# Performance work log

Measured on AMD Instinct MI355X. Metric: run time of the kernel, lower is better.

## Reference

```python
import jax, jax.numpy as jnp
import numpy as np

B, S, D, H = 2, 2048, 1024, 16
HD = D // H
NEG = -10000.0


def setup_inputs() -> dict:
    key = jax.random.key(0)
    ks = jax.random.split(key, 9)
    # xavier-uniform-like scale for square d_model x d_model weights
    lim = float(np.sqrt(6.0 / (D + D)))
    mk_w = lambda k: jax.random.uniform(k, (D, D), jnp.float32, -lim, lim)
    return {
        "q": jax.random.normal(ks[0], (B, S, D), jnp.float32),
        "k": jax.random.normal(ks[1], (B, S, D), jnp.float32),
        "v": jax.random.normal(ks[2], (B, S, D), jnp.float32),
        "attn_mask": jax.random.randint(ks[3], (B, S), 0, 2, jnp.int32),
        "Wq": mk_w(ks[4]),
        "Wk": mk_w(ks[5]),
        "Wv": mk_w(ks[6]),
        "Wo": mk_w(ks[7]),
        "mask_future": 1,
    }


def reference(q, k, v, attn_mask, Wq, Wk, Wv, Wo, mask_future):
    # nn.Linear(bias=False): y = x @ W.T
    def split_heads(x, W):
        return (x @ W.T).reshape(B, S, H, HD).transpose(0, 2, 1, 3)  # [B,H,S,HD]

    qh = split_heads(q, Wq)
    kh = split_heads(k, Wk)
    vh = split_heads(v, Wv)

    scale = 1.0 / np.sqrt(HD)
    scores = jnp.einsum("bhld,bhsd->bhls", qh, kh) * scale  # [B,H,L,S]

    if mask_future:  # static python flag
        rows = jnp.arange(S)[:, None]
        cols = jnp.arange(S)[None, :]
        causal_bias = jnp.where(cols > rows, jnp.float32(NEG), jnp.float32(0.0))
        scores = scores + causal_bias

    # masked_fill(attn_mask == 0, -10000): sets score exactly to NEG (after bias add)
    pad = attn_mask[:, None, None, :]  # [B,1,1,S]
    scores = jnp.where(pad == 0, jnp.float32(NEG), scores)

    probs = jax.nn.softmax(scores, axis=-1)
    ctx = jnp.einsum("bhls,bhsd->bhld", probs, vh)  # [B,H,L,HD]
    ctx = ctx.transpose(0, 2, 1, 3).reshape(B, S, D)
    return ctx @ Wo.T
```

## Files before the change

kernel.cpp:

```cpp
#include <hip/hip_runtime.h>
#include <hip/hip_bf16.h>

typedef __attribute__((ext_vector_type(8))) short bf16x8;
typedef __attribute__((ext_vector_type(4))) short bf16x4;
typedef __attribute__((ext_vector_type(4))) float f32x4;

#define B_ 2
#define S_ 2048
#define D_ 1024
#define H_ 16
#define HD_ 64
#define M_ 4096
#define NEGV (-10000.0f)

#define NQ_ 4194304
#define NW_ 1048576

#if __has_builtin(__builtin_amdgcn_mfma_f32_16x16x16bf16_1k)
#define HAVE_MFMA16 1
#else
#define HAVE_MFMA16 0
#endif

static __device__ __forceinline__ unsigned short f2bf(float x) {
  __hip_bfloat16 h = __float2bfloat16(x);
  return *reinterpret_cast<unsigned short*>(&h);
}

static __device__ __forceinline__ bf16x8 cvt8(const float* p) {
  float4 a = *reinterpret_cast<const float4*>(p);
  float4 b = *reinterpret_cast<const float4*>(p + 4);
  bf16x8 r;
  r[0] = (short)f2bf(a.x); r[1] = (short)f2bf(a.y);
  r[2] = (short)f2bf(a.z); r[3] = (short)f2bf(a.w);
  r[4] = (short)f2bf(b.x); r[5] = (short)f2bf(b.y);
  r[6] = (short)f2bf(b.z); r[7] = (short)f2bf(b.w);
  return r;
}

static __device__ __forceinline__ void gl_lds16(const unsigned short* g, unsigned short* l) {
#if __has_builtin(__builtin_amdgcn_global_load_lds)
  __builtin_amdgcn_global_load_lds(
      (const __attribute__((address_space(1))) unsigned int*)g,
      (__attribute__((address_space(3))) unsigned int*)l, 16, 0, 0);
#else
  *reinterpret_cast<bf16x8*>(l) = *reinterpret_cast<const bf16x8*>(g);
#endif
}


__global__ __launch_bounds__(256) void cvt_all(const float* __restrict__ q,
                                               const float* __restrict__ k,
                                               const float* __restrict__ v,
                                               const float* __restrict__ wq,
                                               const float* __restrict__ wk,
                                               const float* __restrict__ wv,
                                               const float* __restrict__ wo,
                                               unsigned short* __restrict__ dst) {
  for (size_t c = (size_t)blockIdx.x * 256 + threadIdx.x; c < 2097152; c += (size_t)2048 * 256) {
    const size_t e = c * 8;
    const float* s;
    if (e < (size_t)NQ_)            s = q  + e;
    else if (e < (size_t)2 * NQ_)   s = k  + (e - (size_t)NQ_);
    else if (e < (size_t)3 * NQ_)   s = v  + (e - (size_t)2 * NQ_);
    else if (e < (size_t)3 * NQ_ + NW_)     s = wq + (e - (size_t)3 * NQ_);
    else if (e < (size_t)3 * NQ_ + 2 * NW_) s = wk + (e - (size_t)3 * NQ_ - NW_);
    else if (e < (size_t)3 * NQ_ + 3 * NW_) s = wv + (e - (size_t)3 * NQ_ - 2 * NW_);
    else                                    s = wo + (e - (size_t)3 * NQ_ - 3 * NW_);
    *reinterpret_cast<bf16x8*>(dst + e) = cvt8(s);
  }
}

template<bool HSPLIT>
static __device__ __forceinline__ void core_fast(const unsigned short* A,
                                                 const unsigned short* Bw,
                                                 unsigned short* Asm, unsigned short* Bsm,
                                                 int m0, int n0, f32x4 (*acc)[4]) {
  const int tid = threadIdx.x, lane = tid & 63, wid = tid >> 6;
  const int wm = wid >> 1, wn = wid & 1;
  const int l15 = lane & 15, l4 = lane >> 4;

  for (int k0 = 0; k0 < 1024; k0 += 64) {
    __syncthreads();
#pragma unroll
    for (int i = 0; i < 4; ++i) {
      const int idx = tid + 256 * i;
      const int row = idx >> 3;
      const int ce = ((idx & 7) * 8) ^ ((row & 7) << 3);
      const unsigned short* ga;
      if constexpr (HSPLIT) {
        const int m = m0 + row, kk = k0 + ce;
        const int bb = m >> 11, s = m & 2047;
        ga = A + (((size_t)(bb * H_ + (kk >> 6)) * S_ + s) * HD_ + (kk & 63));
      } else {
        ga = A + (size_t)(m0 + row) * 1024 + k0 + ce;
      }
      gl_lds16(ga, Asm + (size_t)idx * 8);
      gl_lds16(Bw + (size_t)(n0 + row) * 1024 + k0 + ce, Bsm + (size_t)idx * 8);
    }
    __syncthreads();
#pragma unroll
    for (int kk = 0; kk < 2; ++kk) {
      bf16x8 af[4], bfr[4];
#pragma unroll
      for (int f = 0; f < 4; ++f) {
        const int ra = wm * 64 + f * 16 + l15;
        const int ca = (kk * 32 + l4 * 8) ^ ((ra & 7) << 3);
        af[f] = *reinterpret_cast<const bf16x8*>(&Asm[ra * 64 + ca]);
        const int rb = wn * 64 + f * 16 + l15;
        const int cb = (kk * 32 + l4 * 8) ^ ((rb & 7) << 3);
        bfr[f] = *reinterpret_cast<const bf16x8*>(&Bsm[rb * 64 + cb]);
      }
#pragma unroll
      for (int fm = 0; fm < 4; ++fm)
#pragma unroll
        for (int fn = 0; fn < 4; ++fn)
          acc[fm][fn] = __builtin_amdgcn_mfma_f32_16x16x32_bf16(af[fm], bfr[fn], acc[fm][fn], 0, 0, 0);
    }
  }
}

__global__ __launch_bounds__(256) void gemm_qkv_fast(const unsigned short* __restrict__ qbf,
                                                     const unsigned short* __restrict__ kbf,
                                                     const unsigned short* __restrict__ vbf,
                                                     const unsigned short* __restrict__ wbf,
                                                     unsigned short* __restrict__ Qh,
                                                     unsigned short* __restrict__ Kh,
                                                     unsigned short* __restrict__ Vt) {
  __shared__ unsigned short Asm[128 * 64];
  __shared__ unsigned short Bsm[128 * 64];
  const int z = blockIdx.z;
  const unsigned short* A  = (z == 0) ? qbf : (z == 1) ? kbf : vbf;
  const unsigned short* Bw = wbf + (size_t)z * NW_;
  const int m0 = blockIdx.y * 128, n0 = blockIdx.x * 128;
  const int lane = threadIdx.x & 63, wid = threadIdx.x >> 6;
  const int wm = wid >> 1, wn = wid & 1;
  const int l15 = lane & 15, l4 = lane >> 4;
  f32x4 acc[4][4] = {};
  core_fast<false>(A, Bw, Asm, Bsm, m0, n0, acc);

#pragma unroll
  for (int fm = 0; fm < 4; ++fm) {
#pragma unroll
    for (int fn = 0; fn < 4; ++fn) {
      const int mg0 = m0 + wm * 64 + fm * 16 + l4 * 4;
      const int ng  = n0 + wn * 64 + fn * 16 + l15;
      const int bidx = mg0 >> 11, s = mg0 & 2047;
      const int h = ng >> 6, d = ng & 63;
      if (z < 2) {
        unsigned short* C = (z == 0) ? Qh : Kh;
#pragma unroll
        for (int r = 0; r < 4; ++r)
          C[((size_t)((bidx * H_ + h) * S_ + s + r)) * HD_ + d] = f2bf(acc[fm][fn][r]);
      } else {
        ushort4 pk;
        pk.x = f2bf(acc[fm][fn][0]); pk.y = f2bf(acc[fm][fn][1]);
        pk.z = f2bf(acc[fm][fn][2]); pk.w = f2bf(acc[fm][fn][3]);
        *reinterpret_cast<ushort4*>(&Vt[((size_t)((bidx * H_ + h) * HD_ + d)) * S_ + s]) = pk;
      }
    }
  }
}

__global__ __launch_bounds__(256) void gemm_o_fast(const unsigned short* __restrict__ ctx,
                                                   const unsigned short* __restrict__ wobf,
                                                   float* __restrict__ Cout) {
  __shared__ unsigned short Asm[128 * 64];
  __shared__ unsigned short Bsm[128 * 64];
  const int m0 = blockIdx.y * 128, n0 = blockIdx.x * 128;
  const int lane = threadIdx.x & 63, wid = threadIdx.x >> 6;
  const int wm = wid >> 1, wn = wid & 1;
  const int l15 = lane & 15, l4 = lane >> 4;
  f32x4 acc[4][4] = {};
  core_fast<true>(ctx, wobf, Asm, Bsm, m0, n0, acc);

#pragma unroll
  for (int fm = 0; fm < 4; ++fm)
#pragma unroll
    for (int fn = 0; fn < 4; ++fn) {
      const int mg0 = m0 + wm * 64 + fm * 16 + l4 * 4;
      const int ng  = n0 + wn * 64 + fn * 16 + l15;
#pragma unroll
      for (int r = 0; r < 4; ++r)
        Cout[(size_t)(mg0 + r) * 1024 + ng] = acc[fm][fn][r];
    }
}


template<bool AF32, bool BF32, bool HSPLIT>
static __device__ __forceinline__ void gemm_core(const void* Av, const void* Bv,
                                                 unsigned short* Asm, unsigned short* Bsm,
                                                 int m0, int n0, f32x4 (*acc)[4]) {
  constexpr int BK = 64, LDT = 72;
  constexpr int K = 1024;
  const int tid = threadIdx.x;
  const int lane = tid & 63, wid = tid >> 6;
  const int wm = wid >> 1, wn = wid & 1;
  const int l15 = lane & 15, l4 = lane >> 4;

  for (int k0 = 0; k0 < K; k0 += BK) {
    __syncthreads();
#pragma unroll
    for (int i = 0; i < 4; ++i) {
      int idx = tid + 256 * i;
      int row = idx >> 3, k8 = (idx & 7) * 8;
      bf16x8 va, vb;
      if constexpr (AF32) {
        va = cvt8((const float*)Av + (size_t)(m0 + row) * K + k0 + k8);
      } else if constexpr (HSPLIT) {
        const int m = m0 + row, kk = k0 + k8;
        const int bb = m >> 11, s = m & 2047;
        va = *reinterpret_cast<const bf16x8*>(
            (const unsigned short*)Av +
            (((size_t)(bb * H_ + (kk >> 6)) * S_ + s) * HD_ + (kk & 63)));
      } else {
        va = *reinterpret_cast<const bf16x8*>((const unsigned short*)Av + (size_t)(m0 + row) * K + k0 + k8);
      }
      if constexpr (BF32) {
        vb = cvt8((const float*)Bv + (size_t)(n0 + row) * K + k0 + k8);
      } else {
        vb = *reinterpret_cast<const bf16x8*>((const unsigned short*)Bv + (size_t)(n0 + row) * K + k0 + k8);
      }
      *reinterpret_cast<bf16x8*>(&Asm[row * LDT + k8]) = va;
      *reinterpret_cast<bf16x8*>(&Bsm[row * LDT + k8]) = vb;
    }
    __syncthreads();
#pragma unroll
    for (int kk = 0; kk < 2; ++kk) {
      bf16x8 af[4], bfr[4];
#pragma unroll
      for (int f = 0; f < 4; ++f) {
        af[f]  = *reinterpret_cast<const bf16x8*>(&Asm[(wm * 64 + f * 16 + l15) * LDT + kk * 32 + l4 * 8]);
        bfr[f] = *reinterpret_cast<const bf16x8*>(&Bsm[(wn * 64 + f * 16 + l15) * LDT + kk * 32 + l4 * 8]);
      }
#pragma unroll
      for (int fm = 0; fm < 4; ++fm)
#pragma unroll
        for (int fn = 0; fn < 4; ++fn)
          acc[fm][fn] = __builtin_amdgcn_mfma_f32_16x16x32_bf16(af[fm], bfr[fn], acc[fm][fn], 0, 0, 0);
    }
  }
}

__global__ __launch_bounds__(256) void gemm_qkv3(const float* __restrict__ q,
                                                 const float* __restrict__ k,
                                                 const float* __restrict__ v,
                                                 const float* __restrict__ Wq,
                                                 const float* __restrict__ Wk,
                                                 const float* __restrict__ Wv,
                                                 unsigned short* __restrict__ Qh,
                                                 unsigned short* __restrict__ Kh,
                                                 unsigned short* __restrict__ Vt) {
  constexpr int LDT = 72;
  __shared__ unsigned short Asm[128 * LDT];
  __shared__ unsigned short Bsm[128 * LDT];
  const int z = blockIdx.z;
  const float* A  = (z == 0) ? q  : (z == 1) ? k  : v;
  const float* Bw = (z == 0) ? Wq : (z == 1) ? Wk : Wv;
  const int m0 = blockIdx.y * 128, n0 = blockIdx.x * 128;
  const int lane = threadIdx.x & 63, wid = threadIdx.x >> 6;
  const int wm = wid >> 1, wn = wid & 1;
  const int l15 = lane & 15, l4 = lane >> 4;
  f32x4 acc[4][4] = {};
  gemm_core<true, true, false>(A, Bw, Asm, Bsm, m0, n0, acc);

#pragma unroll
  for (int fm = 0; fm < 4; ++fm) {
#pragma unroll
    for (int fn = 0; fn < 4; ++fn) {
      const int mg0 = m0 + wm * 64 + fm * 16 + l4 * 4;
      const int ng  = n0 + wn * 64 + fn * 16 + l15;
      const int bidx = mg0 >> 11, s = mg0 & 2047;
      const int h = ng >> 6, d = ng & 63;
      if (z < 2) {
        unsigned short* C = (z == 0) ? Qh : Kh;
#pragma unroll
        for (int r = 0; r < 4; ++r)
          C[((size_t)((bidx * H_ + h) * S_ + s + r)) * HD_ + d] = f2bf(acc[fm][fn][r]);
      } else {
        ushort4 pk;
        pk.x = f2bf(acc[fm][fn][0]); pk.y = f2bf(acc[fm][fn][1]);
        pk.z = f2bf(acc[fm][fn][2]); pk.w = f2bf(acc[fm][fn][3]);
        *reinterpret_cast<ushort4*>(&Vt[((size_t)((bidx * H_ + h) * HD_ + d)) * S_ + s]) = pk;
      }
    }
  }
}

__global__ __launch_bounds__(256) void gemm_oproj(const void* __restrict__ Av,
                                                  const void* __restrict__ Bv,
                                                  float* __restrict__ Cout) {
  constexpr int LDT = 72;
  __shared__ unsigned short Asm[128 * LDT];
  __shared__ unsigned short Bsm[128 * LDT];
  const int m0 = blockIdx.y * 128, n0 = blockIdx.x * 128;
  const int lane = threadIdx.x & 63, wid = threadIdx.x >> 6;
  const int wm = wid >> 1, wn = wid & 1;
  const int l15 = lane & 15, l4 = lane >> 4;
  f32x4 acc[4][4] = {};
  gemm_core<false, true, true>(Av, Bv, Asm, Bsm, m0, n0, acc);

#pragma unroll
  for (int fm = 0; fm < 4; ++fm)
#pragma unroll
    for (int fn = 0; fn < 4; ++fn) {
      const int mg0 = m0 + wm * 64 + fm * 16 + l4 * 4;
      const int ng  = n0 + wn * 64 + fn * 16 + l15;
#pragma unroll
      for (int r = 0; r < 4; ++r)
        Cout[(size_t)(mg0 + r) * 1024 + ng] = acc[fm][fn][r];
    }
}

__global__ __launch_bounds__(128) void attn_fwd(const unsigned short* Qh,
                                                const unsigned short* __restrict__ Kh,
                                                const unsigned short* __restrict__ Vt,
                                                const int* __restrict__ attn_mask,
                                                const int* __restrict__ mask_future,
                                                unsigned short* ctx) {
  constexpr int KVB = 64;
  __shared__ unsigned short Ksm[64 * 64];
  __shared__ unsigned short Vsm[64 * 64];
#if !HAVE_MFMA16
  __shared__ unsigned short Psm[2][16 * 72];
#endif
  __shared__ int s_any;
  const int tid = threadIdx.x, lane = tid & 63, wid = tid >> 6;
  const int l15 = lane & 15, l4 = lane >> 4;
  const int bh = blockIdx.y, b = bh >> 4;
  const int q0 = (int)((blockIdx.x + 9 * blockIdx.y) & 31) * 64;
  const bool causal = (mask_future[0] != 0);
  const int* mrow = attn_mask + b * S_;

  if (tid == 0) s_any = 0;
  __syncthreads();
  for (int i = tid; i <= q0; i += 128)
    if (mrow[i]) s_any = 1;
  __syncthreads();
  const int kb_end = (causal && s_any) ? (q0 + 64) : S_;

  const unsigned short* Qb = Qh + (size_t)bh * S_ * HD_;
  const unsigned short* Kb = Kh + (size_t)bh * S_ * HD_;
  const unsigned short* Vb = Vt + (size_t)bh * HD_ * S_;

  int qrow[2];
  bf16x8 qf0[2], qf1[2];
#pragma unroll
  for (int f = 0; f < 2; ++f) {
    qrow[f] = q0 + wid * 32 + f * 16 + l15;
    qf0[f] = *reinterpret_cast<const bf16x8*>(&Qb[(size_t)qrow[f] * HD_ + l4 * 8]);
    qf1[f] = *reinterpret_cast<const bf16x8*>(&Qb[(size_t)qrow[f] * HD_ + 32 + l4 * 8]);
  }

  float m_run[2] = {-1e30f, -1e30f}, l_run[2] = {0.f, 0.f};
  f32x4 o[2][4] = {};

  bf16x8 kreg[4], vreg[4];
#pragma unroll
  for (int j = 0; j < 4; ++j) {
    const int idx = tid + 128 * j;
    const int row = idx >> 3;
    const int ce = ((idx & 7) * 8) ^ ((row & 7) << 3);
    kreg[j] = *reinterpret_cast<const bf16x8*>(&Kb[(size_t)row * HD_ + ce]);
    vreg[j] = *reinterpret_cast<const bf16x8*>(&Vb[(size_t)row * S_ + ce]);
  }

  for (int kb = 0; kb < kb_end; kb += KVB) {
    __syncthreads();
#pragma unroll
    for (int j = 0; j < 4; ++j) {
      const int idx = tid + 128 * j;
      *reinterpret_cast<bf16x8*>(&Ksm[idx * 8]) = kreg[j];
      *reinterpret_cast<bf16x8*>(&Vsm[idx * 8]) = vreg[j];
    }
    __syncthreads();

    if (kb + KVB < kb_end) {
      const int kn = kb + KVB;
#pragma unroll
      for (int j = 0; j < 4; ++j) {
        const int idx = tid + 128 * j;
        const int row = idx >> 3;
        const int ce = ((idx & 7) * 8) ^ ((row & 7) << 3);
        kreg[j] = *reinterpret_cast<const bf16x8*>(&Kb[(size_t)(kn + row) * HD_ + ce]);
        vreg[j] = *reinterpret_cast<const bf16x8*>(&Vb[(size_t)row * S_ + kn + ce]);
      }
    }

    int4 mk4[4];
#pragma unroll
    for (int nf = 0; nf < 4; ++nf)
      mk4[nf] = *reinterpret_cast<const int4*>(&mrow[kb + nf * 16 + l4 * 4]);

#pragma unroll
    for (int f = 0; f < 2; ++f) {
      f32x4 sc[4];
#pragma unroll
      for (int nf = 0; nf < 4; ++nf) {
        const int ra = nf * 16 + l15, sw = (ra & 7) << 3;
        bf16x8 kf0 = *reinterpret_cast<const bf16x8*>(&Ksm[ra * 64 + ((l4 * 8) ^ sw)]);
        bf16x8 kf1 = *reinterpret_cast<const bf16x8*>(&Ksm[ra * 64 + ((32 + l4 * 8) ^ sw)]);
        f32x4 z = {};
        z = __builtin_amdgcn_mfma_f32_16x16x32_bf16(kf0, qf0[f], z, 0, 0, 0);
        z = __builtin_amdgcn_mfma_f32_16x16x32_bf16(kf1, qf1[f], z, 0, 0, 0);
        sc[nf] = z;
      }

      float p[4][4];
      float mx = -1e30f;
#pragma unroll
      for (int nf = 0; nf < 4; ++nf) {
        const int kbase = kb + nf * 16 + l4 * 4;
#pragma unroll
        for (int r = 0; r < 4; ++r) {
          float vv = sc[nf][r] * 0.125f;
          if (causal && (kbase + r) > qrow[f]) vv += NEGV;
          const int mkr = (r == 0) ? mk4[nf].x : (r == 1) ? mk4[nf].y : (r == 2) ? mk4[nf].z : mk4[nf].w;
          if (mkr == 0) vv = NEGV;
          p[nf][r] = vv;
          mx = fmaxf(mx, vv);
        }
      }
      mx = fmaxf(mx, __shfl_xor(mx, 16));
      mx = fmaxf(mx, __shfl_xor(mx, 32));

      if (__any(mx > m_run[f] + 8.0f)) {
        const float m_new = fmaxf(m_run[f], mx);
        const float scale = __expf(m_run[f] - m_new);
        l_run[f] *= scale;
        float sq[4];
#pragma unroll
        for (int r = 0; r < 4; ++r) sq[r] = __shfl(scale, l4 * 4 + r);
#pragma unroll
        for (int nf2 = 0; nf2 < 4; ++nf2)
#pragma unroll
          for (int r = 0; r < 4; ++r) o[f][nf2][r] *= sq[r];
        m_run[f] = m_new;
      }

      float s_loc = 0.f;
#pragma unroll
      for (int nf = 0; nf < 4; ++nf)
#pragma unroll
        for (int r = 0; r < 4; ++r) {
          float e = __expf(p[nf][r] - m_run[f]);
          p[nf][r] = e;
          s_loc += e;
        }
      s_loc += __shfl_xor(s_loc, 16);
      s_loc += __shfl_xor(s_loc, 32);
      l_run[f] += s_loc;

#if HAVE_MFMA16
      bf16x4 pk[4];
#pragma unroll
      for (int nf = 0; nf < 4; ++nf) {
        bf16x4 t;
        t[0] = (short)f2bf(p[nf][0]); t[1] = (short)f2bf(p[nf][1]);
        t[2] = (short)f2bf(p[nf][2]); t[3] = (short)f2bf(p[nf][3]);
        pk[nf] = t;
      }
#pragma unroll
      for (int nf2 = 0; nf2 < 4; ++nf2) {
        const int rv = nf2 * 16 + l15, swv = (rv & 7) << 3;
#pragma unroll
        for (int nf = 0; nf < 4; ++nf) {
          bf16x4 vf = *reinterpret_cast<const bf16x4*>(&Vsm[rv * 64 + ((nf * 16 + l4 * 4) ^ swv)]);
          o[f][nf2] = __builtin_amdgcn_mfma_f32_16x16x16bf16_1k(pk[nf], vf, o[f][nf2], 0, 0, 0);
        }
      }
#else
      unsigned short* Pw = &Psm[wid][0];
#pragma unroll
      for (int nf = 0; nf < 4; ++nf)
#pragma unroll
        for (int r = 0; r < 4; ++r)
          Pw[l15 * 72 + nf * 16 + l4 * 4 + r] = f2bf(p[nf][r]);
#pragma unroll
      for (int nf2 = 0; nf2 < 4; ++nf2) {
        const int rv = nf2 * 16 + l15, swv = (rv & 7) << 3;
#pragma unroll
        for (int kk = 0; kk < 2; ++kk) {
          bf16x8 pf = *reinterpret_cast<const bf16x8*>(&Pw[l15 * 72 + kk * 32 + l4 * 8]);
          bf16x8 vf = *reinterpret_cast<const bf16x8*>(&Vsm[rv * 64 + ((kk * 32 + l4 * 8) ^ swv)]);
          o[f][nf2] = __builtin_amdgcn_mfma_f32_16x16x32_bf16(pf, vf, o[f][nf2], 0, 0, 0);
        }
      }
#endif
    }
  }

#pragma unroll
  for (int f = 0; f < 2; ++f) {
    const float linv = 1.f / l_run[f];
    float lq[4];
#pragma unroll
    for (int r = 0; r < 4; ++r) lq[r] = __shfl(linv, l4 * 4 + r);
#pragma unroll
    for (int nf2 = 0; nf2 < 4; ++nf2)
#pragma unroll
      for (int r = 0; r < 4; ++r) {
        const int rowg = q0 + wid * 32 + f * 16 + l4 * 4 + r;
        ctx[((size_t)bh * S_ + rowg) * HD_ + nf2 * 16 + l15] = f2bf(o[f][nf2][r] * lq[r]);
      }
  }
}

extern "C" void kernel_launch(void* const* d_in, const int* in_sizes, int n_in,
                              void* d_out, int out_size, void* d_ws, size_t ws_size,
                              hipStream_t stream) {
  const float* q = (const float*)d_in[0];
  const float* k = (const float*)d_in[1];
  const float* v = (const float*)d_in[2];
  const int* attn_mask = (const int*)d_in[3];
  const float* Wq = (const float*)d_in[4];
  const float* Wk = (const float*)d_in[5];
  const float* Wv = (const float*)d_in[6];
  const float* Wo = (const float*)d_in[7];
  const int* mask_future = (const int*)d_in[8];

  unsigned short* ws = (unsigned short*)d_ws;
  unsigned short* Vt = (unsigned short*)d_out;
  float* out = (float*)d_out;
  (void)in_sizes; (void)n_in; (void)out_size;

  const size_t CVT_ELEMS = (size_t)3 * NQ_ + 4 * NW_;
  const size_t NEED = (CVT_ELEMS + 2 * (size_t)NQ_) * 2;

  if (ws_size >= NEED) {
    unsigned short* cvt = ws;
    unsigned short* qbf = cvt;
    unsigned short* kbf = cvt + (size_t)NQ_;
    unsigned short* vbf = cvt + (size_t)2 * NQ_;
    unsigned short* wbf = cvt + (size_t)3 * NQ_;
    unsigned short* Qh  = cvt + CVT_ELEMS;
    unsigned short* Kh  = Qh + (size_t)NQ_;

    cvt_all<<<2048, 256, 0, stream>>>(q, k, v, Wq, Wk, Wv, Wo, cvt);
    gemm_qkv_fast<<<dim3(8, 32, 3), 256, 0, stream>>>(qbf, kbf, vbf, wbf, Qh, Kh, Vt);
    attn_fwd<<<dim3(32, 32), 128, 0, stream>>>(Qh, Kh, Vt, attn_mask, mask_future, Qh);
    gemm_o_fast<<<dim3(8, 32), 256, 0, stream>>>(Qh, wbf + (size_t)3 * NW_, out);
  } else {
    unsigned short* Qh = ws;
    unsigned short* Kh = ws + (size_t)NQ_;
    gemm_qkv3<<<dim3(8, 32, 3), 256, 0, stream>>>(q, k, v, Wq, Wk, Wv, Qh, Kh, Vt);
    attn_fwd<<<dim3(32, 32), 128, 0, stream>>>(Qh, Kh, Vt, attn_mask, mask_future, Qh);
    gemm_oproj<<<dim3(8, 32), 256, 0, stream>>>(Qh, Wo, out);
  }
}
```

Baseline: 175.1 us.

## Enlarge attention query tile to 128 rows and narrow O-projection N tile

The attention kernel now runs 256 threads (four waves) per block over a 128-row query tile, so each K/V block staged in shared memory is reused by twice as many query rows. The grid shrinks to 16 tiles per head, with an XOR-based tile permutation to spread causal work across blocks. The output-projection GEMM now uses a 128x64 tile with its own inlined load/MFMA loop, doubling the block count so more CUs get work. The trade-off is that the larger causal tile does more masked work on the diagonal, and fewer, larger attention blocks lower occupancy flexibility. The non-MFMA16 fallback path was also changed to call the 16x16x16 intrinsic, which may not compile where that intrinsic is absent.

```diff
diff --git a/kernel.cpp b/kernel.cpp
--- a/kernel.cpp
+++ b/kernel.cpp
@@ -166,23 +166,65 @@
                                                    const unsigned short* __restrict__ wobf,
                                                    float* __restrict__ Cout) {
   __shared__ unsigned short Asm[128 * 64];
-  __shared__ unsigned short Bsm[128 * 64];
-  const int m0 = blockIdx.y * 128, n0 = blockIdx.x * 128;
-  const int lane = threadIdx.x & 63, wid = threadIdx.x >> 6;
-  const int wm = wid >> 1, wn = wid & 1;
-  const int l15 = lane & 15, l4 = lane >> 4;
-  f32x4 acc[4][4] = {};
-  core_fast<true>(ctx, wobf, Asm, Bsm, m0, n0, acc);
-
-#pragma unroll
-  for (int fm = 0; fm < 4; ++fm)
+  __shared__ unsigned short Bsm[64 * 64];
+  const int m0 = blockIdx.y * 128, n0 = blockIdx.x * 64;
+  const int tid = threadIdx.x;
+  const int lane = tid & 63, wid = tid >> 6;
+  const int l15 = lane & 15, l4 = lane >> 4;
+  f32x4 acc[2][4] = {};
+
+  for (int k0 = 0; k0 < 1024; k0 += 64) {
+    __syncthreads();
+#pragma unroll
+    for (int i = 0; i < 4; ++i) {
+      const int idx = tid + 256 * i;
+      const int row = idx >> 3;
+      const int ce = ((idx & 7) * 8) ^ ((row & 7) << 3);
+      const int m = m0 + row, kk = k0 + ce;
+      const int bb = m >> 11, s = m & 2047;
+      gl_lds16(ctx + (((size_t)(bb * H_ + (kk >> 6)) * S_ + s) * HD_ + (kk & 63)),
+               Asm + (size_t)idx * 8);
+    }
+#pragma unroll
+    for (int i = 0; i < 2; ++i) {
+      const int idx = tid + 256 * i;
+      const int row = idx >> 3;
+      const int ce = ((idx & 7) * 8) ^ ((row & 7) << 3);
+      gl_lds16(wobf + (size_t)(n0 + row) * 1024 + k0 + ce, Bsm + (size_t)idx * 8);
+    }
+    __syncthreads();
+#pragma unroll
+    for (int kk = 0; kk < 2; ++kk) {
+      bf16x8 af[2], bfr[4];
+#pragma unroll
+      for (int f = 0; f < 2; ++f) {
+        const int ra = wid * 32 + f * 16 + l15;
+        const int ca = (kk * 32 + l4 * 8) ^ ((ra & 7) << 3);
+        af[f] = *reinterpret_cast<const bf16x8*>(&Asm[ra * 64 + ca]);
+      }
+#pragma unroll
+      for (int fn = 0; fn < 4; ++fn) {
+        const int rb = fn * 16 + l15;
+        const int cb = (kk * 32 + l4 * 8) ^ ((rb & 7) << 3);
+        bfr[fn] = *reinterpret_cast<const bf16x8*>(&Bsm[rb * 64 + cb]);
+      }
+#pragma unroll
+      for (int f = 0; f < 2; ++f)
+#pragma unroll
+        for (int fn = 0; fn < 4; ++fn)
+          acc[f][fn] = __builtin_amdgcn_mfma_f32_16x16x32_bf16(af[f], bfr[fn], acc[f][fn], 0, 0, 0);
+    }
+  }
+
+#pragma unroll
+  for (int f = 0; f < 2; ++f)
 #pragma unroll
     for (int fn = 0; fn < 4; ++fn) {
-      const int mg0 = m0 + wm * 64 + fm * 16 + l4 * 4;
-      const int ng  = n0 + wn * 64 + fn * 16 + l15;
+      const int mg0 = m0 + wid * 32 + f * 16 + l4 * 4;
+      const int ng  = n0 + fn * 16 + l15;
 #pragma unroll
       for (int r = 0; r < 4; ++r)
-        Cout[(size_t)(mg0 + r) * 1024 + ng] = acc[fm][fn][r];
+        Cout[(size_t)(mg0 + r) * 1024 + ng] = acc[f][fn][r];
     }
 }
 
@@ -312,7 +354,7 @@
     }
 }
 
-__global__ __launch_bounds__(128) void attn_fwd(const unsigned short* Qh,
+__global__ __launch_bounds__(256) void attn_fwd(const unsigned short* Qh,
                                                 const unsigned short* __restrict__ Kh,
                                                 const unsigned short* __restrict__ Vt,
                                                 const int* __restrict__ attn_mask,
@@ -321,23 +363,21 @@
   constexpr int KVB = 64;
   __shared__ unsigned short Ksm[64 * 64];
   __shared__ unsigned short Vsm[64 * 64];
-#if !HAVE_MFMA16
-  __shared__ unsigned short Psm[2][16 * 72];
-#endif
   __shared__ int s_any;
   const int tid = threadIdx.x, lane = tid & 63, wid = tid >> 6;
   const int l15 = lane & 15, l4 = lane >> 4;
   const int bh = blockIdx.y, b = bh >> 4;
-  const int q0 = (int)((blockIdx.x + 9 * blockIdx.y) & 31) * 64;
+  const int tile = ((int)blockIdx.x ^ (15 * ((int)blockIdx.y >> 4))) & 15;
+  const int q0 = tile * 128;
   const bool causal = (mask_future[0] != 0);
   const int* mrow = attn_mask + b * S_;
 
   if (tid == 0) s_any = 0;
   __syncthreads();
-  for (int i = tid; i <= q0; i += 128)
+  for (int i = tid; i <= q0; i += 256)
     if (mrow[i]) s_any = 1;
   __syncthreads();
-  const int kb_end = (causal && s_any) ? (q0 + 64) : S_;
+  const int kb_end = (causal && s_any) ? (q0 + 128) : S_;
 
   const unsigned short* Qb = Qh + (size_t)bh * S_ * HD_;
   const unsigned short* Kb = Kh + (size_t)bh * S_ * HD_;
@@ -355,10 +395,10 @@
   float m_run[2] = {-1e30f, -1e30f}, l_run[2] = {0.f, 0.f};
   f32x4 o[2][4] = {};
 
-  bf16x8 kreg[4], vreg[4];
-#pragma unroll
-  for (int j = 0; j < 4; ++j) {
-    const int idx = tid + 128 * j;
+  bf16x8 kreg[2], vreg[2];
+#pragma unroll
+  for (int j = 0; j < 2; ++j) {
+    const int idx = tid + 256 * j;
     const int row = idx >> 3;
     const int ce = ((idx & 7) * 8) ^ ((row & 7) << 3);
     kreg[j] = *reinterpret_cast<const bf16x8*>(&Kb[(size_t)row * HD_ + ce]);
@@ -368,8 +408,8 @@
   for (int kb = 0; kb < kb_end; kb += KVB) {
     __syncthreads();
 #pragma unroll
-    for (int j = 0; j < 4; ++j) {
-      const int idx = tid + 128 * j;
+    for (int j = 0; j < 2; ++j) {
+      const int idx = tid + 256 * j;
       *reinterpret_cast<bf16x8*>(&Ksm[idx * 8]) = kreg[j];
       *reinterpret_cast<bf16x8*>(&Vsm[idx * 8]) = vreg[j];
     }
@@ -378,8 +418,8 @@
     if (kb + KVB < kb_end) {
       const int kn = kb + KVB;
 #pragma unroll
-      for (int j = 0; j < 4; ++j) {
-        const int idx = tid + 128 * j;
+      for (int j = 0; j < 2; ++j) {
+        const int idx = tid + 256 * j;
         const int row = idx >> 3;
         const int ce = ((idx & 7) * 8) ^ ((row & 7) << 3);
         kreg[j] = *reinterpret_cast<const bf16x8*>(&Kb[(size_t)(kn + row) * HD_ + ce]);
@@ -470,20 +510,21 @@
         }
       }
 #else
-      unsigned short* Pw = &Psm[wid][0];
-#pragma unroll
-      for (int nf = 0; nf < 4; ++nf)
-#pragma unroll
-        for (int r = 0; r < 4; ++r)
-          Pw[l15 * 72 + nf * 16 + l4 * 4 + r] = f2bf(p[nf][r]);
+      bf16x4 pk[4];
+#pragma unroll
+      for (int nf = 0; nf < 4; ++nf) {
+        bf16x4 t;
+        t[0] = (short)f2bf(p[nf][0]); t[1] = (short)f2bf(p[nf][1]);
+        t[2] = (short)f2bf(p[nf][2]); t[3] = (short)f2bf(p[nf][3]);
+        pk[nf] = t;
+      }
 #pragma unroll
       for (int nf2 = 0; nf2 < 4; ++nf2) {
         const int rv = nf2 * 16 + l15, swv = (rv & 7) << 3;
 #pragma unroll
-        for (int kk = 0; kk < 2; ++kk) {
-          bf16x8 pf = *reinterpret_cast<const bf16x8*>(&Pw[l15 * 72 + kk * 32 + l4 * 8]);
-          bf16x8 vf = *reinterpret_cast<const bf16x8*>(&Vsm[rv * 64 + ((kk * 32 + l4 * 8) ^ swv)]);
-          o[f][nf2] = __builtin_amdgcn_mfma_f32_16x16x32_bf16(pf, vf, o[f][nf2], 0, 0, 0);
+        for (int nf = 0; nf < 4; ++nf) {
+          bf16x4 vf = *reinterpret_cast<const bf16x4*>(&Vsm[rv * 64 + ((nf * 16 + l4 * 4) ^ swv)]);
+          o[f][nf2] = __builtin_amdgcn_mfma_f32_16x16x16bf16_1k(pk[nf], vf, o[f][nf2], 0, 0, 0);
         }
       }
 #endif
@@ -538,13 +579,13 @@
 
     cvt_all<<<2048, 256, 0, stream>>>(q, k, v, Wq, Wk, Wv, Wo, cvt);
     gemm_qkv_fast<<<dim3(8, 32, 3), 256, 0, stream>>>(qbf, kbf, vbf, wbf, Qh, Kh, Vt);
-    attn_fwd<<<dim3(32, 32), 128, 0, stream>>>(Qh, Kh, Vt, attn_mask, mask_future, Qh);
-    gemm_o_fast<<<dim3(8, 32), 256, 0, stream>>>(Qh, wbf + (size_t)3 * NW_, out);
+    attn_fwd<<<dim3(16, 32), 256, 0, stream>>>(Qh, Kh, Vt, attn_mask, mask_future, Qh);
+    gemm_o_fast<<<dim3(16, 32), 256, 0, stream>>>(Qh, wbf + (size_t)3 * NW_, out);
   } else {
     unsigned short* Qh = ws;
     unsigned short* Kh = ws + (size_t)NQ_;
     gemm_qkv3<<<dim3(8, 32, 3), 256, 0, stream>>>(q, k, v, Wq, Wk, Wv, Qh, Kh, Vt);
-    attn_fwd<<<dim3(32, 32), 128, 0, stream>>>(Qh, Kh, Vt, attn_mask, mask_future, Qh);
+    attn_fwd<<<dim3(16, 32), 256, 0, stream>>>(Qh, Kh, Vt, attn_mask, mask_future, Qh);
     gemm_oproj<<<dim3(8, 32), 256, 0, stream>>>(Qh, Wo, out);
   }
 }
```

New measurement: 174.3 us. No clear change (-0.4%).
